# Kernel tuning notes

Measured on AMD Instinct MI355X. Metric: run time of the kernel, lower is better.

The kernel has to match this reference:

```python
import jax, jax.numpy as jnp
import numpy as np

B, T, C, H, HS = 128, 256, 384, 6, 64

def setup_inputs() -> dict:
    key = jax.random.key(0)
    k1, k2, k3, k4, k5 = jax.random.split(key, 5)
    s = 0.02
    return {
        "x": jax.random.normal(k1, (B, T, C), dtype=jnp.float32),
        "Wq": jax.random.normal(k2, (H, C, HS), dtype=jnp.float32) * s,
        "Wk": jax.random.normal(k3, (H, C, HS), dtype=jnp.float32) * s,
        "Wv": jax.random.normal(k4, (H, C, HS), dtype=jnp.float32) * s,
        "Wp": jax.random.normal(k5, (C, C), dtype=jnp.float32) * s,
        "bp": jnp.zeros((C,), dtype=jnp.float32),
    }

def reference(x, Wq, Wk, Wv, Wp, bp):
    # per-head projections: [B,H,T,HS]
    q = jnp.einsum('btc,hcd->bhtd', x, Wq)
    k = jnp.einsum('btc,hcd->bhtd', x, Wk)
    v = jnp.einsum('btc,hcd->bhtd', x, Wv)
    scale = 1.0 / jnp.sqrt(jnp.asarray(HS, dtype=x.dtype))
    # scores: [B,H,T,T], causal mask then stable softmax
    scores = jnp.einsum('bhtd,bhsd->bhts', q, k) * scale
    causal = jnp.tril(jnp.ones((T, T), dtype=bool))
    scores = jnp.where(causal, scores, -jnp.inf)
    wei = jax.nn.softmax(scores, axis=-1)
    # dropout is identity in eval mode
    out = jnp.einsum('bhts,bhsd->bhtd', wei, v)  # [B,H,T,HS]
    out = out.transpose(0, 2, 1, 3).reshape(B, T, H * HS)  # concat heads
    return out @ Wp.T + bp  # output projection
```

## Files before the change

kernel.cpp:

```cpp
#include <hip/hip_runtime.h>
#include <hip/hip_bf16.h>
#include <math.h>

#define B_   128
#define T_   256
#define C_   384
#define H_   6
#define HS_  64
#define NTOK (B_*T_)
#define NQKV (3*C_)

typedef unsigned short u16;
typedef __attribute__((ext_vector_type(8))) short bf16x8;
typedef __attribute__((ext_vector_type(4))) float f32x4;

__device__ __forceinline__ u16 f2b(float f) {
    unsigned int u = __builtin_bit_cast(unsigned int, f);
    unsigned int r = (u + 0x7FFFu + ((u >> 16) & 1u)) >> 16;
    return (u16)r;
}

__device__ __forceinline__ void gl2lds16(const u16* g, u16* l) {
    __builtin_amdgcn_global_load_lds(
        (const __attribute__((address_space(1))) unsigned int*)g,
        (__attribute__((address_space(3))) unsigned int*)l, 16, 0, 0);
}

#define J0_ (NTOK*C_/8)
#define J2_ (C_*C_/8)
#define J1_ (NQKV*C_)

__global__ __launch_bounds__(256) void prep(
    const float* __restrict__ x,  const float* __restrict__ Wq,
    const float* __restrict__ Wk, const float* __restrict__ Wv,
    const float* __restrict__ Wp,
    u16* __restrict__ xb, u16* __restrict__ wct, u16* __restrict__ wpb)
{
    int i = blockIdx.x * 256 + threadIdx.x;
    if (i < J0_) {
        const float4* s = (const float4*)x + (size_t)i * 2;
        float4 a = s[0], b = s[1];
        ushort4 o1, o2;
        o1.x = f2b(a.x); o1.y = f2b(a.y); o1.z = f2b(a.z); o1.w = f2b(a.w);
        o2.x = f2b(b.x); o2.y = f2b(b.y); o2.z = f2b(b.z); o2.w = f2b(b.w);
        ((ushort4*)xb)[(size_t)i * 2]     = o1;
        ((ushort4*)xb)[(size_t)i * 2 + 1] = o2;
    } else if (i < J0_ + J2_) {
        int j = i - J0_;
        const float4* s = (const float4*)Wp + (size_t)j * 2;
        float4 a = s[0], b = s[1];
        ushort4 o1, o2;
        o1.x = f2b(a.x); o1.y = f2b(a.y); o1.z = f2b(a.z); o1.w = f2b(a.w);
        o2.x = f2b(b.x); o2.y = f2b(b.y); o2.z = f2b(b.z); o2.w = f2b(b.w);
        ((ushort4*)wpb)[(size_t)j * 2]     = o1;
        ((ushort4*)wpb)[(size_t)j * 2 + 1] = o2;
    } else {
        int j = i - J0_ - J2_;
        if (j < J1_) {
            int n = j / C_, c = j % C_;
            int p = n / C_, rem = n % C_;
            int h = rem >> 6, d = rem & 63;
            const float* W = (p == 0 ? Wq : (p == 1 ? Wk : Wv));
            wct[j] = f2b(W[(h * C_ + c) * HS_ + d]);
        }
    }
}

__global__ __launch_bounds__(256) void gemm_qkv(
    const u16* __restrict__ xb, const u16* __restrict__ wct,
    u16* __restrict__ qo, u16* __restrict__ ko, u16* __restrict__ vt)
{
    __shared__ __align__(16) u16 As[128 * 64];
    __shared__ __align__(16) u16 Bs[128 * 64];

    const int tid = threadIdx.x;
    const int m0g = blockIdx.x * 128;
    const int n0g = blockIdx.y * 128;
    const int w = tid >> 6, lane = tid & 63;
    const int lm = lane & 15, qd = lane >> 4;
    const int wm = (w & 1) * 64, wn = (w >> 1) * 64;

    const int srow   = w * 32 + (lane >> 3);
    const int schunk = (lane & 7) ^ ((lane >> 3) & 7);
    const u16* gA = xb  + (size_t)(m0g + srow) * C_ + schunk * 8;
    const u16* gB = wct + (size_t)(n0g + srow) * C_ + schunk * 8;
    u16* lA = &As[(w * 32) * 64];
    u16* lB = &Bs[(w * 32) * 64];

    f32x4 acc[4][4];
    #pragma unroll
    for (int mi = 0; mi < 4; ++mi)
        #pragma unroll
        for (int ni = 0; ni < 4; ++ni)
            acc[mi][ni] = (f32x4){0.f, 0.f, 0.f, 0.f};

    for (int k0 = 0; k0 < C_; k0 += 64) {
        __syncthreads();
        #pragma unroll
        for (int j = 0; j < 4; ++j) {
            gl2lds16(gA + j * 8 * C_, lA + j * 8 * 64);
            gl2lds16(gB + j * 8 * C_, lB + j * 8 * 64);
        }
        gA += 64; gB += 64;
        __syncthreads();

        #pragma unroll
        for (int ks = 0; ks < 2; ++ks) {
            bf16x8 af[4], bfr[4];
            #pragma unroll
            for (int mi = 0; mi < 4; ++mi) {
                const int row = wm + mi * 16 + lm;
                const int sl = (ks * 4 + qd) ^ (lm & 7);
                af[mi] = *(const bf16x8*)&As[row * 64 + sl * 8];
            }
            #pragma unroll
            for (int ni = 0; ni < 4; ++ni) {
                const int row = wn + ni * 16 + lm;
                const int sl = (ks * 4 + qd) ^ (lm & 7);
                bfr[ni] = *(const bf16x8*)&Bs[row * 64 + sl * 8];
            }
            #pragma unroll
            for (int mi = 0; mi < 4; ++mi)
                #pragma unroll
                for (int ni = 0; ni < 4; ++ni)
                    acc[mi][ni] = __builtin_amdgcn_mfma_f32_16x16x32_bf16(
                        af[mi], bfr[ni], acc[mi][ni], 0, 0, 0);
        }
    }

    const int bI = m0g >> 8;
    const int tBase = (m0g & 255) + wm;
    const int yb_ = blockIdx.y;

    if (yb_ < 6) {
        u16* dst = (yb_ < 3) ? qo : ko;
        const float scl = (yb_ < 3) ? 0.125f : 1.0f;
        #pragma unroll
        for (int mi = 0; mi < 4; ++mi) {
            #pragma unroll
            for (int ni = 0; ni < 4; ++ni) {
                const int nn = n0g + wn + ni * 16 + lm - ((yb_ < 3) ? 0 : 384);
                const int h = nn >> 6, d = nn & 63;
                #pragma unroll
                for (int r = 0; r < 4; ++r) {
                    const int t = tBase + mi * 16 + qd * 4 + r;
                    dst[((size_t)(bI * H_ + h) * T_ + t) * HS_ + d]
                        = f2b(acc[mi][ni][r] * scl);
                }
            }
        }
    } else {
        #pragma unroll
        for (int mi = 0; mi < 4; ++mi) {
            #pragma unroll
            for (int ni = 0; ni < 4; ++ni) {
                const int nn = n0g + wn + ni * 16 + lm - 768;
                const int h = nn >> 6, d = nn & 63;
                const int t0 = tBase + mi * 16 + qd * 4;
                ushort4 sv;
                sv.x = f2b(acc[mi][ni][0]); sv.y = f2b(acc[mi][ni][1]);
                sv.z = f2b(acc[mi][ni][2]); sv.w = f2b(acc[mi][ni][3]);
                *(ushort4*)(vt + ((size_t)(bI * H_ + h) * HS_ + d) * T_ + t0) = sv;
            }
        }
    }
}

__global__ __launch_bounds__(256) void attn_mfma(
    const u16* __restrict__ q, const u16* __restrict__ k,
    const u16* __restrict__ vt, u16* __restrict__ yb)
{
    __shared__ __align__(16) u16 Ks[64 * 64];
    __shared__ __align__(16) u16 Vs[64 * 64];
    __shared__ __align__(16) u16 Ps[4][2][16 * 72];

    const int bh = blockIdx.x;
    const int qt = blockIdx.y;
    const int b = bh / H_, h = bh % H_;
    const int tid = threadIdx.x, w = tid >> 6, lane = tid & 63;
    const int lm = lane & 15, qd = lane >> 4;

    const u16* qb = q  + (size_t)bh * T_ * HS_;
    const u16* kb = k  + (size_t)bh * T_ * HS_;
    const u16* vb = vt + (size_t)bh * HS_ * T_;

    const int t0 = qt * 128 + w * 16;

    bf16x8 aq[2][2];
    #pragma unroll
    for (int rg = 0; rg < 2; ++rg) {
        const u16* qrow = qb + (size_t)(t0 + rg * 64 + lm) * HS_;
        aq[rg][0] = *(const bf16x8*)(qrow + qd * 8);
        aq[rg][1] = *(const bf16x8*)(qrow + 32 + qd * 8);
    }

    f32x4 acc[2][4];
    float ms[2][4], ls[2][4];
    #pragma unroll
    for (int rg = 0; rg < 2; ++rg) {
        #pragma unroll
        for (int ni = 0; ni < 4; ++ni) acc[rg][ni] = (f32x4){0.f, 0.f, 0.f, 0.f};
        #pragma unroll
        for (int r = 0; r < 4; ++r) { ms[rg][r] = -INFINITY; ls[rg][r] = 0.f; }
    }

    const int srow   = w * 16 + (lane >> 3);
    const int schunk = (lane & 7) ^ ((lane >> 3) & 7);
    const u16* gK = kb + (size_t)srow * HS_ + schunk * 8;
    const u16* gV = vb + (size_t)srow * T_  + schunk * 8;
    u16* lK = &Ks[(w * 16) * 64];
    u16* lV = &Vs[(w * 16) * 64];

    const int nkt = (qt + 1) * 2;
    for (int kt = 0; kt < nkt; ++kt) {
        const int j0 = kt * 64;
        __syncthreads();
        #pragma unroll
        for (int j = 0; j < 2; ++j) {
            gl2lds16(gK + j * 8 * HS_, lK + j * 8 * 64);
            gl2lds16(gV + j * 8 * T_,  lV + j * 8 * 64);
        }
        gK += (size_t)64 * HS_;
        gV += 64;
        __syncthreads();

        #pragma unroll
        for (int rg = 0; rg < 2; ++rg) {
            const int trg = t0 + rg * 64;
            if (j0 > trg + 15) continue;
            const bool needmask = (j0 + 63 > trg);

            f32x4 st[4];
            #pragma unroll
            for (int ni = 0; ni < 4; ++ni) st[ni] = (f32x4){0.f, 0.f, 0.f, 0.f};
            #pragma unroll
            for (int ks = 0; ks < 2; ++ks) {
                #pragma unroll
                for (int ni = 0; ni < 4; ++ni) {
                    const int sl = (ks * 4 + qd) ^ (lm & 7);
                    bf16x8 bk = *(const bf16x8*)&Ks[(ni * 16 + lm) * 64 + sl * 8];
                    st[ni] = __builtin_amdgcn_mfma_f32_16x16x32_bf16(
                        aq[rg][ks], bk, st[ni], 0, 0, 0);
                }
            }

            float vals[4][4], rowmax[4];
            #pragma unroll
            for (int r = 0; r < 4; ++r) rowmax[r] = -INFINITY;
            #pragma unroll
            for (int ni = 0; ni < 4; ++ni) {
                const int s_g = j0 + ni * 16 + lm;
                #pragma unroll
                for (int r = 0; r < 4; ++r) {
                    float sc = st[ni][r];
                    if (needmask) {
                        const int t_g = trg + qd * 4 + r;
                        sc = (s_g > t_g) ? -1e30f : sc;
                    }
                    vals[ni][r] = sc;
                    rowmax[r] = fmaxf(rowmax[r], sc);
                }
            }
            #pragma unroll
            for (int msk = 1; msk <= 8; msk <<= 1)
                #pragma unroll
                for (int r = 0; r < 4; ++r)
                    rowmax[r] = fmaxf(rowmax[r], __shfl_xor(rowmax[r], msk, 64));

            float corr[4], rowsum[4];
            #pragma unroll
            for (int r = 0; r < 4; ++r) {
                const float mn = fmaxf(ms[rg][r], rowmax[r]);
                corr[r] = __expf(ms[rg][r] - mn);
                ms[rg][r] = mn;
                rowsum[r] = 0.f;
            }
            u16* Pw = &Ps[w][rg][0];
            #pragma unroll
            for (int ni = 0; ni < 4; ++ni) {
                #pragma unroll
                for (int r = 0; r < 4; ++r) {
                    const float p = __expf(vals[ni][r] - ms[rg][r]);
                    rowsum[r] += p;
                    Pw[(qd * 4 + r) * 72 + ni * 16 + lm] = f2b(p);
                }
            }
            #pragma unroll
            for (int msk = 1; msk <= 8; msk <<= 1)
                #pragma unroll
                for (int r = 0; r < 4; ++r)
                    rowsum[r] += __shfl_xor(rowsum[r], msk, 64);
            #pragma unroll
            for (int r = 0; r < 4; ++r) ls[rg][r] = ls[rg][r] * corr[r] + rowsum[r];
            #pragma unroll
            for (int ni = 0; ni < 4; ++ni)
                #pragma unroll
                for (int r = 0; r < 4; ++r)
                    acc[rg][ni][r] *= corr[r];

            #pragma unroll
            for (int ks = 0; ks < 2; ++ks) {
                bf16x8 pa = *(const bf16x8*)&Pw[lm * 72 + ks * 32 + qd * 8];
                #pragma unroll
                for (int ni = 0; ni < 4; ++ni) {
                    const int sl = (ks * 4 + qd) ^ (lm & 7);
                    bf16x8 bv = *(const bf16x8*)&Vs[(ni * 16 + lm) * 64 + sl * 8];
                    acc[rg][ni] = __builtin_amdgcn_mfma_f32_16x16x32_bf16(
                        pa, bv, acc[rg][ni], 0, 0, 0);
                }
            }
        }
    }

    #pragma unroll
    for (int rg = 0; rg < 2; ++rg) {
        #pragma unroll
        for (int r = 0; r < 4; ++r) {
            const float inv = 1.f / ls[rg][r];
            const int t_g = t0 + rg * 64 + qd * 4 + r;
            #pragma unroll
            for (int ni = 0; ni < 4; ++ni) {
                const int col = h * HS_ + ni * 16 + lm;
                yb[((size_t)(b * T_ + t_g)) * C_ + col] = f2b(acc[rg][ni][r] * inv);
            }
        }
    }
}

__global__ __launch_bounds__(256) void gemm_proj(
    const u16* __restrict__ yb, const u16* __restrict__ wpb,
    const float* __restrict__ bp, float* __restrict__ out)
{
    __shared__ __align__(16) u16 As[128 * 64];
    __shared__ __align__(16) u16 Bs[128 * 64];

    const int tid = threadIdx.x;
    const int m0g = blockIdx.x * 128;
    const int n0g = blockIdx.y * 128;
    const int w = tid >> 6, lane = tid & 63;
    const int lm = lane & 15, qd = lane >> 4;
    const int wm = (w & 1) * 64, wn = (w >> 1) * 64;

    const int srow   = w * 32 + (lane >> 3);
    const int schunk = (lane & 7) ^ ((lane >> 3) & 7);
    const u16* gA = yb  + (size_t)(m0g + srow) * C_ + schunk * 8;
    const u16* gB = wpb + (size_t)(n0g + srow) * C_ + schunk * 8;
    u16* lA = &As[(w * 32) * 64];
    u16* lB = &Bs[(w * 32) * 64];

    f32x4 acc[4][4];
    #pragma unroll
    for (int mi = 0; mi < 4; ++mi)
        #pragma unroll
        for (int ni = 0; ni < 4; ++ni)
            acc[mi][ni] = (f32x4){0.f, 0.f, 0.f, 0.f};

    for (int k0 = 0; k0 < C_; k0 += 64) {
        __syncthreads();
        #pragma unroll
        for (int j = 0; j < 4; ++j) {
            gl2lds16(gA + j * 8 * C_, lA + j * 8 * 64);
            gl2lds16(gB + j * 8 * C_, lB + j * 8 * 64);
        }
        gA += 64; gB += 64;
        __syncthreads();

        #pragma unroll
        for (int ks = 0; ks < 2; ++ks) {
            bf16x8 af[4], bfr[4];
            #pragma unroll
            for (int mi = 0; mi < 4; ++mi) {
                const int row = wm + mi * 16 + lm;
                const int sl = (ks * 4 + qd) ^ (lm & 7);
                af[mi] = *(const bf16x8*)&As[row * 64 + sl * 8];
            }
            #pragma unroll
            for (int ni = 0; ni < 4; ++ni) {
                const int row = wn + ni * 16 + lm;
                const int sl = (ks * 4 + qd) ^ (lm & 7);
                bfr[ni] = *(const bf16x8*)&Bs[row * 64 + sl * 8];
            }
            #pragma unroll
            for (int mi = 0; mi < 4; ++mi)
                #pragma unroll
                for (int ni = 0; ni < 4; ++ni)
                    acc[mi][ni] = __builtin_amdgcn_mfma_f32_16x16x32_bf16(
                        af[mi], bfr[ni], acc[mi][ni], 0, 0, 0);
        }
    }

    #pragma unroll
    for (int mi = 0; mi < 4; ++mi) {
        #pragma unroll
        for (int ni = 0; ni < 4; ++ni) {
            const int n = n0g + wn + ni * 16 + lm;
            const float bpv = bp[n];
            #pragma unroll
            for (int r = 0; r < 4; ++r) {
                const int m = m0g + wm + mi * 16 + qd * 4 + r;
                out[(size_t)m * C_ + n] = acc[mi][ni][r] + bpv;
            }
        }
    }
}

extern "C" void kernel_launch(void* const* d_in, const int* in_sizes, int n_in,
                              void* d_out, int out_size, void* d_ws, size_t ws_size,
                              hipStream_t stream)
{
    const float* x  = (const float*)d_in[0];
    const float* Wq = (const float*)d_in[1];
    const float* Wk = (const float*)d_in[2];
    const float* Wv = (const float*)d_in[3];
    const float* Wp = (const float*)d_in[4];
    const float* bp = (const float*)d_in[5];
    float* out = (float*)d_out;

    u16* xb  = (u16*)d_ws;
    u16* wct = xb  + (size_t)NTOK * C_;
    u16* wpb = wct + (size_t)NQKV * C_;
    u16* qo  = wpb + (size_t)C_ * C_;
    u16* ko  = qo  + (size_t)B_ * H_ * T_ * HS_;
    u16* vt  = ko  + (size_t)B_ * H_ * T_ * HS_;
    u16* yb  = vt  + (size_t)B_ * H_ * T_ * HS_;

    const int prep_blocks = (J0_ + J2_ + J1_ + 255) / 256;
    hipLaunchKernelGGL(prep, dim3(prep_blocks), dim3(256), 0, stream,
                       x, Wq, Wk, Wv, Wp, xb, wct, wpb);

    hipLaunchKernelGGL(gemm_qkv, dim3(NTOK / 128, NQKV / 128), dim3(256), 0, stream,
                       xb, wct, qo, ko, vt);

    hipLaunchKernelGGL(attn_mfma, dim3(B_ * H_, T_ / 128), dim3(256), 0, stream,
                       qo, ko, vt, yb);

    hipLaunchKernelGGL(gemm_proj, dim3(NTOK / 128, C_ / 128), dim3(256), 0, stream,
                       yb, wpb, bp, out);
}
```

Before: 212.7 us.

## Coalesce GEMM/attention epilogues via LDS, preload full K/V, use exp2 softmax

The QKV and projection GEMMs now stage their output tiles through LDS so they can write 16-byte coalesced rows, and their grids become 1D with column-fastest block order so blocks sharing an A tile run close together. The attention kernel loads all of K and V for a (batch, head) into LDS once, with XOR swizzles, which removes the per-tile barriers and loads. Its output is also transposed through LDS for coalesced stores. The softmax switches to exp2, with log2(e) folded into the Q scale. The trade-off is more LDS per attention block (roughly 70KB), which lowers occupancy, plus extra barriers in the GEMM epilogues.

```diff
diff --git a/kernel.cpp b/kernel.cpp
--- a/kernel.cpp
+++ b/kernel.cpp
@@ -20,11 +20,21 @@
     return (u16)r;
 }
 
+__device__ __forceinline__ float fexp2(float x) {
+#if __has_builtin(__builtin_amdgcn_exp2f)
+    return __builtin_amdgcn_exp2f(x);
+#else
+    return exp2f(x);
+#endif
+}
+
 __device__ __forceinline__ void gl2lds16(const u16* g, u16* l) {
     __builtin_amdgcn_global_load_lds(
         (const __attribute__((address_space(1))) unsigned int*)g,
         (__attribute__((address_space(3))) unsigned int*)l, 16, 0, 0);
 }
+
+#define QSCALE 0.180336880f
 
 #define J0_ (NTOK*C_/8)
 #define J2_ (C_*C_/8)
@@ -73,9 +83,13 @@
     __shared__ __align__(16) u16 As[128 * 64];
     __shared__ __align__(16) u16 Bs[128 * 64];
 
+    const int gid  = blockIdx.x;
+    const int colb = gid % 9;
+    const int rowb = gid / 9;
+    const int m0g  = rowb * 128;
+    const int n0g  = colb * 128;
+
     const int tid = threadIdx.x;
-    const int m0g = blockIdx.x * 128;
-    const int n0g = blockIdx.y * 128;
     const int w = tid >> 6, lane = tid & 63;
     const int lm = lane & 15, qd = lane >> 4;
     const int wm = (w & 1) * 64, wn = (w >> 1) * 64;
@@ -129,34 +143,42 @@
     }
 
     const int bI = m0g >> 8;
-    const int tBase = (m0g & 255) + wm;
-    const int yb_ = blockIdx.y;
-
-    if (yb_ < 6) {
-        u16* dst = (yb_ < 3) ? qo : ko;
-        const float scl = (yb_ < 3) ? 0.125f : 1.0f;
+    const int tBase = m0g & 255;
+
+    if (colb < 6) {
+        u16* dst = (colb < 3) ? qo : ko;
+        const float scl = (colb < 3) ? QSCALE : 1.0f;
+        const int hBase = (colb % 3) * 2;
+        u16 (*tb)[140] = (u16(*)[140])As;
+        const int rloc = tid >> 3;
+        const int mg   = rloc >> 4;
         #pragma unroll
         for (int mi = 0; mi < 4; ++mi) {
+            __syncthreads();
+            #pragma unroll
+            for (int ni = 0; ni < 4; ++ni)
+                #pragma unroll
+                for (int r = 0; r < 4; ++r)
+                    tb[(w & 1) * 16 + qd * 4 + r][wn + ni * 16 + lm]
+                        = f2b(acc[mi][ni][r] * scl);
+            __syncthreads();
+            const int t = tBase + mg * 64 + mi * 16 + (rloc & 15);
+            #pragma unroll
+            for (int j = 0; j < 2; ++j) {
+                const int col = (tid & 7) * 8 + j * 64;
+                const int h = hBase + (col >> 6);
+                bf16x8 vv = *(const bf16x8*)&tb[rloc][col];
+                *(bf16x8*)(dst + ((size_t)(bI * H_ + h) * T_ + t) * HS_ + (col & 63)) = vv;
+            }
+        }
+    } else {
+        #pragma unroll
+        for (int mi = 0; mi < 4; ++mi) {
             #pragma unroll
             for (int ni = 0; ni < 4; ++ni) {
-                const int nn = n0g + wn + ni * 16 + lm - ((yb_ < 3) ? 0 : 384);
+                const int nn = (colb - 6) * 128 + wn + ni * 16 + lm;
                 const int h = nn >> 6, d = nn & 63;
-                #pragma unroll
-                for (int r = 0; r < 4; ++r) {
-                    const int t = tBase + mi * 16 + qd * 4 + r;
-                    dst[((size_t)(bI * H_ + h) * T_ + t) * HS_ + d]
-                        = f2b(acc[mi][ni][r] * scl);
-                }
-            }
-        }
-    } else {
-        #pragma unroll
-        for (int mi = 0; mi < 4; ++mi) {
-            #pragma unroll
-            for (int ni = 0; ni < 4; ++ni) {
-                const int nn = n0g + wn + ni * 16 + lm - 768;
-                const int h = nn >> 6, d = nn & 63;
-                const int t0 = tBase + mi * 16 + qd * 4;
+                const int t0 = tBase + wm + mi * 16 + qd * 4;
                 ushort4 sv;
                 sv.x = f2b(acc[mi][ni][0]); sv.y = f2b(acc[mi][ni][1]);
                 sv.z = f2b(acc[mi][ni][2]); sv.w = f2b(acc[mi][ni][3]);
@@ -170,9 +192,9 @@
     const u16* __restrict__ q, const u16* __restrict__ k,
     const u16* __restrict__ vt, u16* __restrict__ yb)
 {
-    __shared__ __align__(16) u16 Ks[64 * 64];
-    __shared__ __align__(16) u16 Vs[64 * 64];
-    __shared__ __align__(16) u16 Ps[4][2][16 * 72];
+    __shared__ __align__(16) u16 Ks[256 * 64];
+    __shared__ __align__(16) u16 Vs[64 * 256];
+    __shared__ __align__(16) u16 Ps[4][16 * 72];
 
     const int bh = blockIdx.x;
     const int qt = blockIdx.y;
@@ -194,6 +216,22 @@
         aq[rg][1] = *(const bf16x8*)(qrow + 32 + qd * 8);
     }
 
+    #pragma unroll
+    for (int j = 0; j < 8; ++j) {
+        {
+            const int L = (j * 4 + w) * 64 + lane;
+            const int row = L >> 3;
+            const int c = (L & 7) ^ (row & 7);
+            gl2lds16(kb + (size_t)row * HS_ + c * 8, &Ks[(size_t)(j * 4 + w) * 512]);
+        }
+        {
+            const int L = (j * 4 + w) * 64 + lane;
+            const int d = L >> 5;
+            const int c = (L & 31) ^ (d & 15);
+            gl2lds16(vb + (size_t)d * T_ + c * 8, &Vs[(size_t)(j * 4 + w) * 512]);
+        }
+    }
+
     f32x4 acc[2][4];
     float ms[2][4], ls[2][4];
     #pragma unroll
@@ -204,26 +242,12 @@
         for (int r = 0; r < 4; ++r) { ms[rg][r] = -INFINITY; ls[rg][r] = 0.f; }
     }
 
-    const int srow   = w * 16 + (lane >> 3);
-    const int schunk = (lane & 7) ^ ((lane >> 3) & 7);
-    const u16* gK = kb + (size_t)srow * HS_ + schunk * 8;
-    const u16* gV = vb + (size_t)srow * T_  + schunk * 8;
-    u16* lK = &Ks[(w * 16) * 64];
-    u16* lV = &Vs[(w * 16) * 64];
-
+    __syncthreads();
+
+    u16* Pw = &Ps[w][0];
     const int nkt = (qt + 1) * 2;
     for (int kt = 0; kt < nkt; ++kt) {
         const int j0 = kt * 64;
-        __syncthreads();
-        #pragma unroll
-        for (int j = 0; j < 2; ++j) {
-            gl2lds16(gK + j * 8 * HS_, lK + j * 8 * 64);
-            gl2lds16(gV + j * 8 * T_,  lV + j * 8 * 64);
-        }
-        gK += (size_t)64 * HS_;
-        gV += 64;
-        __syncthreads();
-
         #pragma unroll
         for (int rg = 0; rg < 2; ++rg) {
             const int trg = t0 + rg * 64;
@@ -237,8 +261,9 @@
             for (int ks = 0; ks < 2; ++ks) {
                 #pragma unroll
                 for (int ni = 0; ni < 4; ++ni) {
+                    const int row = j0 + ni * 16 + lm;
                     const int sl = (ks * 4 + qd) ^ (lm & 7);
-                    bf16x8 bk = *(const bf16x8*)&Ks[(ni * 16 + lm) * 64 + sl * 8];
+                    bf16x8 bk = *(const bf16x8*)&Ks[row * 64 + sl * 8];
                     st[ni] = __builtin_amdgcn_mfma_f32_16x16x32_bf16(
                         aq[rg][ks], bk, st[ni], 0, 0, 0);
                 }
@@ -271,16 +296,15 @@
             #pragma unroll
             for (int r = 0; r < 4; ++r) {
                 const float mn = fmaxf(ms[rg][r], rowmax[r]);
-                corr[r] = __expf(ms[rg][r] - mn);
+                corr[r] = fexp2(ms[rg][r] - mn);
                 ms[rg][r] = mn;
                 rowsum[r] = 0.f;
             }
-            u16* Pw = &Ps[w][rg][0];
             #pragma unroll
             for (int ni = 0; ni < 4; ++ni) {
                 #pragma unroll
                 for (int r = 0; r < 4; ++r) {
-                    const float p = __expf(vals[ni][r] - ms[rg][r]);
+                    const float p = fexp2(vals[ni][r] - ms[rg][r]);
                     rowsum[r] += p;
                     Pw[(qd * 4 + r) * 72 + ni * 16 + lm] = f2b(p);
                 }
@@ -303,8 +327,9 @@
                 bf16x8 pa = *(const bf16x8*)&Pw[lm * 72 + ks * 32 + qd * 8];
                 #pragma unroll
                 for (int ni = 0; ni < 4; ++ni) {
-                    const int sl = (ks * 4 + qd) ^ (lm & 7);
-                    bf16x8 bv = *(const bf16x8*)&Vs[(ni * 16 + lm) * 64 + sl * 8];
+                    const int d = ni * 16 + lm;
+                    const int c = ((j0 >> 3) + ks * 4 + qd) ^ lm;
+                    bf16x8 bv = *(const bf16x8*)&Vs[d * 256 + c * 8];
                     acc[rg][ni] = __builtin_amdgcn_mfma_f32_16x16x32_bf16(
                         pa, bv, acc[rg][ni], 0, 0, 0);
                 }
@@ -312,18 +337,26 @@
         }
     }
 
-    #pragma unroll
-    for (int rg = 0; rg < 2; ++rg) {
+    __syncthreads();
+    u16 (*yt)[72] = (u16(*)[72])Ks;
+    #pragma unroll
+    for (int rg = 0; rg < 2; ++rg)
         #pragma unroll
         for (int r = 0; r < 4; ++r) {
             const float inv = 1.f / ls[rg][r];
-            const int t_g = t0 + rg * 64 + qd * 4 + r;
-            #pragma unroll
-            for (int ni = 0; ni < 4; ++ni) {
-                const int col = h * HS_ + ni * 16 + lm;
-                yb[((size_t)(b * T_ + t_g)) * C_ + col] = f2b(acc[rg][ni][r] * inv);
-            }
-        }
+            #pragma unroll
+            for (int ni = 0; ni < 4; ++ni)
+                yt[w * 16 + rg * 64 + qd * 4 + r][ni * 16 + lm]
+                    = f2b(acc[rg][ni][r] * inv);
+        }
+    __syncthreads();
+    #pragma unroll
+    for (int rr = 0; rr < 4; ++rr) {
+        const int row = rr * 32 + (tid >> 3);
+        const int col = (tid & 7) * 8;
+        bf16x8 vv = *(const bf16x8*)&yt[row][col];
+        const int t_g = qt * 128 + row;
+        *(bf16x8*)(yb + ((size_t)(b * T_ + t_g)) * C_ + h * 64 + col) = vv;
     }
 }
 
@@ -331,12 +364,17 @@
     const u16* __restrict__ yb, const u16* __restrict__ wpb,
     const float* __restrict__ bp, float* __restrict__ out)
 {
-    __shared__ __align__(16) u16 As[128 * 64];
-    __shared__ __align__(16) u16 Bs[128 * 64];
+    __shared__ __align__(16) u16 SMEM[128 * 64 * 2];
+    u16* As = SMEM;
+    u16* Bs = SMEM + 128 * 64;
+
+    const int gid  = blockIdx.x;
+    const int colb = gid % 3;
+    const int rowb = gid / 3;
+    const int m0g  = rowb * 128;
+    const int n0g  = colb * 128;
 
     const int tid = threadIdx.x;
-    const int m0g = blockIdx.x * 128;
-    const int n0g = blockIdx.y * 128;
     const int w = tid >> 6, lane = tid & 63;
     const int lm = lane & 15, qd = lane >> 4;
     const int wm = (w & 1) * 64, wn = (w >> 1) * 64;
@@ -389,17 +427,29 @@
         }
     }
 
+    float bpv[4];
+    #pragma unroll
+    for (int ni = 0; ni < 4; ++ni) bpv[ni] = bp[n0g + wn + ni * 16 + lm];
+
+    float (*tb)[134] = (float(*)[134])SMEM;
+    const int rloc = tid >> 3;
+    const int mg   = rloc >> 4;
     #pragma unroll
     for (int mi = 0; mi < 4; ++mi) {
-        #pragma unroll
-        for (int ni = 0; ni < 4; ++ni) {
-            const int n = n0g + wn + ni * 16 + lm;
-            const float bpv = bp[n];
-            #pragma unroll
-            for (int r = 0; r < 4; ++r) {
-                const int m = m0g + wm + mi * 16 + qd * 4 + r;
-                out[(size_t)m * C_ + n] = acc[mi][ni][r] + bpv;
-            }
+        __syncthreads();
+        #pragma unroll
+        for (int ni = 0; ni < 4; ++ni)
+            #pragma unroll
+            for (int r = 0; r < 4; ++r)
+                tb[(w & 1) * 16 + qd * 4 + r][wn + ni * 16 + lm]
+                    = acc[mi][ni][r] + bpv[ni];
+        __syncthreads();
+        const int m = m0g + mg * 64 + mi * 16 + (rloc & 15);
+        #pragma unroll
+        for (int j = 0; j < 4; ++j) {
+            const int col = (tid & 7) * 4 + j * 32;
+            float4 vv = *(const float4*)&tb[rloc][col];
+            *(float4*)(out + (size_t)m * C_ + n0g + col) = vv;
         }
     }
 }
@@ -428,12 +478,12 @@
     hipLaunchKernelGGL(prep, dim3(prep_blocks), dim3(256), 0, stream,
                        x, Wq, Wk, Wv, Wp, xb, wct, wpb);
 
-    hipLaunchKernelGGL(gemm_qkv, dim3(NTOK / 128, NQKV / 128), dim3(256), 0, stream,
+    hipLaunchKernelGGL(gemm_qkv, dim3(NTOK / 128 * (NQKV / 128)), dim3(256), 0, stream,
                        xb, wct, qo, ko, vt);
 
     hipLaunchKernelGGL(attn_mfma, dim3(B_ * H_, T_ / 128), dim3(256), 0, stream,
                        qo, ko, vt, yb);
 
-    hipLaunchKernelGGL(gemm_proj, dim3(NTOK / 128, C_ / 128), dim3(256), 0, stream,
+    hipLaunchKernelGGL(gemm_proj, dim3(NTOK / 128 * (C_ / 128)), dim3(256), 0, stream,
                        yb, wpb, bp, out);
 }
```

Result: slower. 229.9 us (+8.1%).
